# Performance work log

Hardware: AMD Instinct MI355X
Metric: run time of the kernel (lower is better)

Reference implementation:

```python
import jax, jax.numpy as jnp
import numpy as np
import math

B, S, H, NH, HD = 2, 2048, 4096, 32, 128  # batch, seq, hidden, heads, head_dim
ROPE_BASE = 10000.0


def setup_inputs() -> dict:
    key = jax.random.key(0)
    k1, k2 = jax.random.split(key)
    hidden_states = jax.random.normal(k1, (B, S, H), jnp.float32) * 0.02
    W_pack = jax.random.normal(k2, (3 * H, H), jnp.float32) * (1.0 / math.sqrt(H))
    position_ids = jnp.tile(jnp.arange(S, dtype=jnp.int64)[None, :], (B, 1))
    # 4D additive causal mask, as passed by HF Baichuan to this attention module
    causal = jnp.triu(jnp.full((S, S), -1e9, jnp.float32), 1)[None, None, :, :]
    return {"hidden_states": hidden_states, "W_pack": W_pack,
            "attention_mask": causal, "position_ids": position_ids}


def _rope(x, position_ids):
    # x: [B, S, NH, HD]; NeoX-style rotate-half RoPE over full head_dim
    half = HD // 2
    inv_freq = 1.0 / (ROPE_BASE ** (jnp.arange(half, dtype=jnp.float32) / half))
    ang = position_ids.astype(jnp.float32)[:, :, None] * inv_freq  # [B,S,half]
    cos = jnp.concatenate([jnp.cos(ang), jnp.cos(ang)], axis=-1)[:, :, None, :]
    sin = jnp.concatenate([jnp.sin(ang), jnp.sin(ang)], axis=-1)[:, :, None, :]
    x1, x2 = jnp.split(x, 2, axis=-1)
    x_rot = jnp.concatenate([-x2, x1], axis=-1)
    return x * cos + x_rot * sin


def reference(hidden_states, W_pack, attention_mask, position_ids):
    # fused QKV projection (W_pack has no bias in Baichuan)
    proj = hidden_states @ W_pack.T                      # [B,S,3H]
    q, k, v = jnp.split(proj, 3, axis=-1)
    q = q.reshape(B, S, NH, HD)
    k = k.reshape(B, S, NH, HD)
    v = v.reshape(B, S, NH, HD)
    q = _rope(q, position_ids)
    k = _rope(k, position_ids)
    # scaled dot-product attention
    scale = 1.0 / math.sqrt(HD)
    q = q.transpose(0, 2, 1, 3)  # [B,NH,S,HD]
    k = k.transpose(0, 2, 1, 3)
    v = v.transpose(0, 2, 1, 3)
    scores = jnp.einsum("bhqd,bhkd->bhqk", q, k) * scale + attention_mask
    probs = jax.nn.softmax(scores, axis=-1)
    ctx = jnp.einsum("bhqk,bhkd->bhqd", probs, v)        # [B,NH,S,HD]
    attn_output = ctx.transpose(0, 2, 1, 3).reshape(B, S, H)
    return attn_output
```

## Files before the change

kernel.cpp:

```cpp
#include <hip/hip_runtime.h>
#include <hip/hip_bf16.h>
#include <stdint.h>

typedef unsigned short u16;
typedef __attribute__((ext_vector_type(8))) short s16x8;
typedef __attribute__((ext_vector_type(8))) unsigned short u16x8;
typedef __attribute__((ext_vector_type(4))) unsigned short u16x4;
typedef __attribute__((ext_vector_type(4))) float fx4;
typedef __bf16 bf16x8 __attribute__((ext_vector_type(8)));

#define SEQ 2048
#define HID 4096
#define NHEAD 32
#define HDIM 128
#define P3H 12288
#define NKT 64

__device__ __forceinline__ u16 f2bf(float f) {
  unsigned u = __builtin_bit_cast(unsigned, f);
  u += 0x7fffu + ((u >> 16) & 1u);
  return (u16)(u >> 16);
}
__device__ __forceinline__ float bf2f(u16 h) {
  unsigned u = ((unsigned)h) << 16;
  return __builtin_bit_cast(float, u);
}
__device__ __forceinline__ void gload_lds16(const void* g, void* l) {
  __builtin_amdgcn_global_load_lds((const __attribute__((address_space(1))) void*)g,
                                   (__attribute__((address_space(3))) void*)l, 16, 0, 0);
}
__device__ __forceinline__ fx4 mfma16(s16x8 a, s16x8 b, fx4 c) {
  return __builtin_amdgcn_mfma_f32_16x16x32_bf16(
      __builtin_bit_cast(bf16x8, a), __builtin_bit_cast(bf16x8, b), c, 0, 0, 0);
}

__global__ void k_cvt(const float* __restrict__ src, u16* __restrict__ dst, int n4) {
  int i = blockIdx.x * blockDim.x + threadIdx.x;
  if (i >= n4) return;
  float4 v = reinterpret_cast<const float4*>(src)[i];
  u16x4 o;
  o[0] = f2bf(v.x); o[1] = f2bf(v.y); o[2] = f2bf(v.z); o[3] = f2bf(v.w);
  reinterpret_cast<u16x4*>(dst)[i] = o;
}

__device__ __forceinline__ void stage_half(const u16* __restrict__ g, u16* l, int r0, int t) {
#pragma unroll
  for (int c = 0; c < 2; c++) {
    int row = r0 + c * 64 + (t >> 3);
    int blk = (t & 7) ^ ((t >> 3) & 7);
    gload_lds16(g + (size_t)row * HID + blk * 8, l + row * 64 + (t & 7) * 8);
  }
}

#define BAR_OPEN __builtin_amdgcn_s_barrier()
#define BAR_CLOSE do { __builtin_amdgcn_s_barrier(); __builtin_amdgcn_sched_barrier(0); } while (0)
#define LGKM0 do { asm volatile("s_waitcnt lgkmcnt(0)" ::: "memory"); \
                   __builtin_amdgcn_sched_barrier(0); } while (0)

#define LDA_QUAD(qm) do { \
  _Pragma("unroll") for (int mi = 0; mi < 4; mi++) \
  _Pragma("unroll") for (int ks = 0; ks < 2; ks++) { \
    int row = wrr + (qm) * 64 + mi * 16 + li; \
    aA[mi][ks] = *(const s16x8*)&Al[row * 64 + (((ks * 4 + lg) ^ (row & 7)) << 3)]; \
  } } while (0)

#define LDB_QUAD(qn) do { \
  _Pragma("unroll") for (int ni = 0; ni < 2; ni++) \
  _Pragma("unroll") for (int ks = 0; ks < 2; ks++) { \
    int row = wcc + (qn) * 32 + ni * 16 + li; \
    aB[qn][ni][ks] = *(const s16x8*)&Bl[row * 64 + (((ks * 4 + lg) ^ (row & 7)) << 3)]; \
  } } while (0)

#define MMA_QUAD(qm, qn) do { \
  _Pragma("unroll") for (int ks = 0; ks < 2; ks++) \
  _Pragma("unroll") for (int mi = 0; mi < 4; mi++) \
  _Pragma("unroll") for (int ni = 0; ni < 2; ni++) \
    acc[(qm) * 4 + mi][(qn) * 2 + ni] = \
        mfma16(aA[mi][ks], aB[qn][ni][ks], acc[(qm) * 4 + mi][(qn) * 2 + ni]); \
  } while (0)

__global__ void __launch_bounds__(512, 2) k_gemm_qkv(const u16* __restrict__ A,
                                                     const u16* __restrict__ W,
                                                     u16* __restrict__ C) {
  __shared__ u16 SM[2][2][256 * 64];
  const int t = threadIdx.x;
  const int lane = t & 63;
  const int w = t >> 6;
  const int li = lane & 15, lg = lane >> 4;
  const int wr = w >> 2, wc = w & 3;
  const int wrr = wr * 128, wcc = wc * 64;

  const int cpx = gridDim.x >> 3;
  const int swz = (blockIdx.x & 7) * cpx + (blockIdx.x >> 3);
  const int bm = swz / 48, bn = swz - bm * 48;
  const int m0 = bm * 256, n0 = bn * 256;

  const u16* Ag = A + (size_t)m0 * HID;
  const u16* Wg = W + (size_t)n0 * HID;

  fx4 acc[8][4];
#pragma unroll
  for (int i = 0; i < 8; i++)
#pragma unroll
    for (int j = 0; j < 4; j++) acc[i][j] = fx4{0.f, 0.f, 0.f, 0.f};
  s16x8 aA[4][2], aB[2][2][2];

  stage_half(Ag, &SM[0][0][0], 0, t);
  stage_half(Ag, &SM[0][0][0], 128, t);
  stage_half(Wg, &SM[0][1][0], 0, t);
  stage_half(Wg, &SM[0][1][0], 128, t);
  stage_half(Wg + 64, &SM[1][1][0], 0, t);
  stage_half(Wg + 64, &SM[1][1][0], 128, t);
  stage_half(Ag + 64, &SM[1][0][0], 0, t);
  asm volatile("s_waitcnt vmcnt(6)" ::: "memory");
  BAR_CLOSE;

  for (int kt = 0; kt < NKT; kt++) {
    const int cur = kt & 1;
    u16* Al = &SM[cur][0][0];
    u16* Bl = &SM[cur][1][0];
    u16* Anxt = &SM[cur ^ 1][0][0];
    const u16* Ag1 = Ag + (size_t)(kt + 1) * 64;
    const u16* Ag2 = Ag + (size_t)(kt + 2) * 64;
    const u16* Wg2 = Wg + (size_t)(kt + 2) * 64;

    LDA_QUAD(0);
    LDB_QUAD(0);
    if (kt + 1 < NKT) stage_half(Ag1, Anxt, 128, t);
    asm volatile("s_waitcnt lgkmcnt(8)" ::: "memory");
    BAR_OPEN;
    LGKM0;
    __builtin_amdgcn_s_setprio(1);
    MMA_QUAD(0, 0);
    __builtin_amdgcn_s_setprio(0);
    BAR_CLOSE;

    LDB_QUAD(1);
    BAR_OPEN;
    LGKM0;
    __builtin_amdgcn_s_setprio(1);
    MMA_QUAD(0, 1);
    __builtin_amdgcn_s_setprio(0);
    BAR_CLOSE;

    LDA_QUAD(1);
    if (kt + 2 < NKT) stage_half(Wg2, Bl, 0, t);
    BAR_OPEN;
    LGKM0;
    __builtin_amdgcn_s_setprio(1);
    MMA_QUAD(1, 1);
    __builtin_amdgcn_s_setprio(0);
    BAR_CLOSE;

    if (kt + 2 < NKT) {
      stage_half(Wg2, Bl, 128, t);
      stage_half(Ag2, Al, 0, t);
    }
    BAR_OPEN;
    LGKM0;
    __builtin_amdgcn_s_setprio(1);
    MMA_QUAD(1, 0);
    __builtin_amdgcn_s_setprio(0);
    if (kt + 2 < NKT) {
      asm volatile("s_waitcnt vmcnt(6)" ::: "memory");
    } else {
      asm volatile("s_waitcnt vmcnt(0)" ::: "memory");
    }
    BAR_CLOSE;
  }

#pragma unroll
  for (int mi = 0; mi < 8; mi++)
#pragma unroll
    for (int ni = 0; ni < 4; ni++)
#pragma unroll
      for (int j = 0; j < 4; j++) {
        int r = m0 + wrr + mi * 16 + lg * 4 + j;
        int c = n0 + wcc + ni * 16 + li;
        C[(size_t)r * P3H + c] = f2bf(acc[mi][ni][j]);
      }
}

__global__ void k_rope(const u16* __restrict__ proj, u16* __restrict__ q,
                       u16* __restrict__ k, const int* __restrict__ pos_ids) {
  int t = blockIdx.x * 256 + threadIdx.x;
  int d = t & 63;
  int h = (t >> 6) & 31;
  int s = (t >> 11) & 2047;
  int b = t >> 22;
  int prow = b * SEQ + s;
  const u16* pr = proj + (size_t)prow * P3H;
  float q1 = bf2f(pr[h * HDIM + d]);
  float q2 = bf2f(pr[h * HDIM + d + 64]);
  float k1 = bf2f(pr[HID + h * HDIM + d]);
  float k2 = bf2f(pr[HID + h * HDIM + d + 64]);
  float p = (float)pos_ids[prow];
  float invf = exp2f(-(float)d * 0.2076205059304601f);
  float ang = p * invf;
  float sn, cs;
  sincosf(ang, &sn, &cs);
  size_t base = ((size_t)(b * NHEAD + h) * SEQ + s) * HDIM + d;
  q[base]      = f2bf(q1 * cs - q2 * sn);
  q[base + 64] = f2bf(q2 * cs + q1 * sn);
  k[base]      = f2bf(k1 * cs - k2 * sn);
  k[base + 64] = f2bf(k2 * cs + k1 * sn);
}

__global__ void k_vtrans(const u16* __restrict__ proj, u16* __restrict__ vt) {
  int wid = (blockIdx.x * 256 + threadIdx.x) >> 6;
  int lane = threadIdx.x & 63;
  int half = wid & 1;
  int s8 = (wid >> 1) & 255;
  int h = (wid >> 9) & 31;
  int b = wid >> 14;
  int d = half * 64 + lane;
  int s0 = s8 * 8;
  u16x8 v;
#pragma unroll
  for (int r = 0; r < 8; r++)
    v[r] = proj[(size_t)(b * SEQ + s0 + r) * P3H + 2 * HID + h * HDIM + d];
  *reinterpret_cast<u16x8*>(&vt[((size_t)(b * NHEAD + h) * HDIM + d) * SEQ + s0]) = v;
}

__device__ __forceinline__ void stage_kv(const u16* __restrict__ kp, const u16* __restrict__ vp,
                                         u16* ksl, u16* vsl, int kv0, int t) {
#pragma unroll
  for (int c = 0; c < 4; c++) {
    int row = c * 16 + (t >> 4);
    int cb = (t & 15) ^ (row & 7);
    gload_lds16(kp + (size_t)(kv0 + row) * HDIM + cb * 8, ksl + (size_t)(c * 256 + t) * 8);
  }
#pragma unroll
  for (int c = 0; c < 4; c++) {
    int row = c * 32 + (t >> 3);
    int cb = (t & 7) ^ (row & 7);
    gload_lds16(vp + (size_t)row * SEQ + kv0 + cb * 8, vsl + (size_t)(c * 256 + t) * 8);
  }
}

__global__ void __launch_bounds__(256, 2) k_attn(const u16* __restrict__ q,
                                                 const u16* __restrict__ k,
                                                 const u16* __restrict__ vt,
                                                 float* __restrict__ out) {
  __shared__ u16 Ks[2][64 * 128];
  __shared__ u16 Vs[2][128 * 64];
  __shared__ u16 Ps[4][2][16 * 64];
  const int t = threadIdx.x;
  const int w = t >> 6, lane = t & 63;
  const int li = lane & 15, lg = lane >> 4;
  const int qb = gridDim.x - 1 - blockIdx.x;
  const int h = blockIdx.y, b = blockIdx.z;
  const int q0 = qb * 128;
  const int qw = q0 + w * 32;
  const size_t bh = (size_t)(b * NHEAD + h);
  const u16* qp = q + bh * SEQ * HDIM;
  const u16* kp = k + bh * SEQ * HDIM;
  const u16* vp = vt + bh * HDIM * SEQ;

  s16x8 bq[2][4];
#pragma unroll
  for (int g = 0; g < 2; g++)
#pragma unroll
    for (int kk = 0; kk < 4; kk++)
      bq[g][kk] = *reinterpret_cast<const s16x8*>(
          &qp[(size_t)(qw + g * 16 + li) * HDIM + kk * 32 + lg * 8]);

  fx4 Oacc[2][8];
#pragma unroll
  for (int g = 0; g < 2; g++)
#pragma unroll
    for (int nd = 0; nd < 8; nd++) Oacc[g][nd] = fx4{0.f, 0.f, 0.f, 0.f};
  float mrun[2] = {-1e30f, -1e30f}, lrun[2] = {0.f, 0.f};

  const float SC2 = 0.12752551286084110f;
  const float THR = 8.0f / SC2;
  const int nt = 2 * (qb + 1);
  const int psw = (li & 7) << 4;

  stage_kv(kp, vp, Ks[0], Vs[0], 0, t);

  for (int tk = 0; tk < nt; tk++) {
    const int cur = tk & 1;
    if (tk + 1 < nt) {
      stage_kv(kp, vp, Ks[cur ^ 1], Vs[cur ^ 1], (tk + 1) * 64, t);
      asm volatile("s_waitcnt vmcnt(8)" ::: "memory");
    } else {
      asm volatile("s_waitcnt vmcnt(0)" ::: "memory");
    }
    __builtin_amdgcn_s_barrier();

    const u16* Kc = Ks[cur];
    const u16* Vc = Vs[cur];
    const int kv0 = tk * 64;
    const bool diag = (tk >= 2 * qb);

    fx4 sc[2][4];
#pragma unroll
    for (int g = 0; g < 2; g++)
#pragma unroll
      for (int n = 0; n < 4; n++) sc[g][n] = fx4{0.f, 0.f, 0.f, 0.f};
    __builtin_amdgcn_s_setprio(1);
#pragma unroll
    for (int n = 0; n < 4; n++) {
      int r = n * 16 + li;
#pragma unroll
      for (int kk = 0; kk < 4; kk++) {
        s16x8 ak = *reinterpret_cast<const s16x8*>(
            &Kc[r * 128 + (((kk * 4 + lg) ^ (r & 7)) << 3)]);
        sc[0][n] = mfma16(ak, bq[0][kk], sc[0][n]);
        sc[1][n] = mfma16(ak, bq[1][kk], sc[1][n]);
      }
    }
    __builtin_amdgcn_s_setprio(0);

    if (diag) {
#pragma unroll
      for (int g = 0; g < 2; g++) {
        const int qg = qw + g * 16 + li;
#pragma unroll
        for (int n = 0; n < 4; n++)
#pragma unroll
          for (int j = 0; j < 4; j++) {
            int kvg = kv0 + n * 16 + lg * 4 + j;
            if (kvg > qg) sc[g][n][j] = -1e30f;
          }
      }
    }

    s16x8 ap[2][2];
#pragma unroll
    for (int g = 0; g < 2; g++) {
      float mn[4];
#pragma unroll
      for (int n = 0; n < 4; n++)
        mn[n] = fmaxf(fmaxf(sc[g][n][0], sc[g][n][1]), fmaxf(sc[g][n][2], sc[g][n][3]));
      float vmax = fmaxf(fmaxf(mn[0], mn[1]), fmaxf(mn[2], mn[3]));
      vmax = fmaxf(vmax, __shfl_xor(vmax, 16));
      vmax = fmaxf(vmax, __shfl_xor(vmax, 32));
      if (__any(vmax > mrun[g] + THR)) {
        float mnew = fmaxf(mrun[g], vmax);
        float al = exp2f((mrun[g] - mnew) * SC2);
        mrun[g] = mnew;
        lrun[g] *= al;
        float alj[4];
#pragma unroll
        for (int j = 0; j < 4; j++) alj[j] = __shfl(al, lg * 4 + j);
#pragma unroll
        for (int nd = 0; nd < 8; nd++)
#pragma unroll
          for (int j = 0; j < 4; j++) Oacc[g][nd][j] *= alj[j];
      }
      const float mS = mrun[g] * SC2;
      float ps[4];
#pragma unroll
      for (int n = 0; n < 4; n++) {
        u16x4 pk;
        float pv0 = exp2f(__builtin_fmaf(sc[g][n][0], SC2, -mS));
        float pv1 = exp2f(__builtin_fmaf(sc[g][n][1], SC2, -mS));
        float pv2 = exp2f(__builtin_fmaf(sc[g][n][2], SC2, -mS));
        float pv3 = exp2f(__builtin_fmaf(sc[g][n][3], SC2, -mS));
        pk[0] = __builtin_bit_cast(u16, __float2bfloat16(pv0));
        pk[1] = __builtin_bit_cast(u16, __float2bfloat16(pv1));
        pk[2] = __builtin_bit_cast(u16, __float2bfloat16(pv2));
        pk[3] = __builtin_bit_cast(u16, __float2bfloat16(pv3));
        ps[n] = (pv0 + pv1) + (pv2 + pv3);
        *reinterpret_cast<u16x4*>(
            &Ps[w][g][li * 64 + (((n * 32 + lg * 8) ^ psw) >> 1)]) = pk;
      }
      float psum = (ps[0] + ps[1]) + (ps[2] + ps[3]);
      psum += __shfl_xor(psum, 16);
      psum += __shfl_xor(psum, 32);
      lrun[g] += psum;
#pragma unroll
      for (int kvc = 0; kvc < 2; kvc++)
        ap[g][kvc] = *reinterpret_cast<const s16x8*>(
            &Ps[w][g][li * 64 + (((kvc * 64 + lg * 16) ^ psw) >> 1)]);
    }

    __builtin_amdgcn_s_setprio(1);
#pragma unroll
    for (int nd = 0; nd < 8; nd++) {
      int dr = nd * 16 + li;
#pragma unroll
      for (int kvc = 0; kvc < 2; kvc++) {
        s16x8 bv = *reinterpret_cast<const s16x8*>(
            &Vc[dr * 64 + (((kvc * 4 + lg) ^ (dr & 7)) << 3)]);
        Oacc[0][nd] = mfma16(ap[0][kvc], bv, Oacc[0][nd]);
        Oacc[1][nd] = mfma16(ap[1][kvc], bv, Oacc[1][nd]);
      }
    }
    __builtin_amdgcn_s_setprio(0);

    __builtin_amdgcn_s_barrier();
    __builtin_amdgcn_sched_barrier(0);
  }

#pragma unroll
  for (int g = 0; g < 2; g++)
#pragma unroll
    for (int j = 0; j < 4; j++) {
      float rl = 1.0f / __shfl(lrun[g], lg * 4 + j);
      int s = qw + g * 16 + lg * 4 + j;
      float* op = out + ((size_t)(b * SEQ) + s) * HID + h * HDIM;
#pragma unroll
      for (int nd = 0; nd < 8; nd++) op[nd * 16 + li] = Oacc[g][nd][j] * rl;
    }
}

extern "C" void kernel_launch(void* const* d_in, const int* in_sizes, int n_in,
                              void* d_out, int out_size, void* d_ws, size_t ws_size,
                              hipStream_t stream) {
  const float* hidden = (const float*)d_in[0];
  const float* wpack = (const float*)d_in[1];
  const int* pos = (const int*)d_in[3];
  float* out = (float*)d_out;

  char* ws = (char*)d_ws;
  u16* hid_bf = (u16*)ws;
  u16* wp_bf = (u16*)(ws + ((size_t)32 << 20));
  u16* qb = (u16*)ws;
  u16* kb = (u16*)(ws + ((size_t)32 << 20));
  u16* vtb = (u16*)(ws + ((size_t)64 << 20));
  u16* proj = (u16*)(ws + ((size_t)128 << 20));

  k_cvt<<<(HID * HID / 4 + 255) / 256, 256, 0, stream>>>(hidden, hid_bf, HID * HID / 4);
  k_cvt<<<(P3H * HID / 4 + 255) / 256, 256, 0, stream>>>(wpack, wp_bf, P3H * HID / 4);

  k_gemm_qkv<<<768, 512, 0, stream>>>(hid_bf, wp_bf, proj);

  k_rope<<<(2 * SEQ * NHEAD * 64) / 256, 256, 0, stream>>>(proj, qb, kb, pos);
  k_vtrans<<<(2 * NHEAD * (SEQ / 8) * 2) / 4, 256, 0, stream>>>(proj, vtb);

  dim3 ga(SEQ / 128, NHEAD, 2);
  k_attn<<<ga, 256, 0, stream>>>(qb, kb, vtb, out);
}
```

Before: 645.7 us.

## Read K/V directly from global in attention, reorder grid, retime GEMM A prefetch

The attention kernel drops its double-buffered LDS staging of K and V and its barriers. Each wave now loads its MFMA operands straight from global memory, relying on L1/L2 cache reuse. The grid is reordered so blocks sharing a batch-head launch adjacently, and the GEMM prologue/loop moves the A-tile prefetch one step later with adjusted vmcnt waits. This removes LDS traffic and sync but exposes global-load latency inside the MFMA loops and duplicates K/V reads across the four waves.

```diff
diff --git a/kernel.cpp b/kernel.cpp
--- a/kernel.cpp
+++ b/kernel.cpp
@@ -105,14 +105,13 @@
     for (int j = 0; j < 4; j++) acc[i][j] = fx4{0.f, 0.f, 0.f, 0.f};
   s16x8 aA[4][2], aB[2][2][2];
 
+  stage_half(Wg, &SM[0][1][0], 0, t);
+  stage_half(Wg, &SM[0][1][0], 128, t);
   stage_half(Ag, &SM[0][0][0], 0, t);
   stage_half(Ag, &SM[0][0][0], 128, t);
-  stage_half(Wg, &SM[0][1][0], 0, t);
-  stage_half(Wg, &SM[0][1][0], 128, t);
   stage_half(Wg + 64, &SM[1][1][0], 0, t);
   stage_half(Wg + 64, &SM[1][1][0], 128, t);
-  stage_half(Ag + 64, &SM[1][0][0], 0, t);
-  asm volatile("s_waitcnt vmcnt(6)" ::: "memory");
+  asm volatile("s_waitcnt vmcnt(4)" ::: "memory");
   BAR_CLOSE;
 
   for (int kt = 0; kt < NKT; kt++) {
@@ -120,13 +119,12 @@
     u16* Al = &SM[cur][0][0];
     u16* Bl = &SM[cur][1][0];
     u16* Anxt = &SM[cur ^ 1][0][0];
-    const u16* Ag1 = Ag + (size_t)(kt + 1) * 64;
-    const u16* Ag2 = Ag + (size_t)(kt + 2) * 64;
-    const u16* Wg2 = Wg + (size_t)(kt + 2) * 64;
+    const u16* Agn = Ag + (size_t)(kt + 1) * 64;
+    const u16* Wgn = Wg + (size_t)(kt + 2) * 64;
 
     LDA_QUAD(0);
     LDB_QUAD(0);
-    if (kt + 1 < NKT) stage_half(Ag1, Anxt, 128, t);
+    if (kt + 1 < NKT) stage_half(Agn, Anxt, 0, t);
     asm volatile("s_waitcnt lgkmcnt(8)" ::: "memory");
     BAR_OPEN;
     LGKM0;
@@ -136,6 +134,7 @@
     BAR_CLOSE;
 
     LDB_QUAD(1);
+    if (kt + 1 < NKT) stage_half(Agn, Anxt, 128, t);
     BAR_OPEN;
     LGKM0;
     __builtin_amdgcn_s_setprio(1);
@@ -144,7 +143,7 @@
     BAR_CLOSE;
 
     LDA_QUAD(1);
-    if (kt + 2 < NKT) stage_half(Wg2, Bl, 0, t);
+    if (kt + 2 < NKT) stage_half(Wgn, Bl, 0, t);
     BAR_OPEN;
     LGKM0;
     __builtin_amdgcn_s_setprio(1);
@@ -152,17 +151,14 @@
     __builtin_amdgcn_s_setprio(0);
     BAR_CLOSE;
 
-    if (kt + 2 < NKT) {
-      stage_half(Wg2, Bl, 128, t);
-      stage_half(Ag2, Al, 0, t);
-    }
+    if (kt + 2 < NKT) stage_half(Wgn, Bl, 128, t);
     BAR_OPEN;
     LGKM0;
     __builtin_amdgcn_s_setprio(1);
     MMA_QUAD(1, 0);
     __builtin_amdgcn_s_setprio(0);
     if (kt + 2 < NKT) {
-      asm volatile("s_waitcnt vmcnt(6)" ::: "memory");
+      asm volatile("s_waitcnt vmcnt(4)" ::: "memory");
     } else {
       asm volatile("s_waitcnt vmcnt(0)" ::: "memory");
     }
@@ -222,40 +218,20 @@
   *reinterpret_cast<u16x8*>(&vt[((size_t)(b * NHEAD + h) * HDIM + d) * SEQ + s0]) = v;
 }
 
-__device__ __forceinline__ void stage_kv(const u16* __restrict__ kp, const u16* __restrict__ vp,
-                                         u16* ksl, u16* vsl, int kv0, int t) {
-#pragma unroll
-  for (int c = 0; c < 4; c++) {
-    int row = c * 16 + (t >> 4);
-    int cb = (t & 15) ^ (row & 7);
-    gload_lds16(kp + (size_t)(kv0 + row) * HDIM + cb * 8, ksl + (size_t)(c * 256 + t) * 8);
-  }
-#pragma unroll
-  for (int c = 0; c < 4; c++) {
-    int row = c * 32 + (t >> 3);
-    int cb = (t & 7) ^ (row & 7);
-    gload_lds16(vp + (size_t)row * SEQ + kv0 + cb * 8, vsl + (size_t)(c * 256 + t) * 8);
-  }
-}
-
-__global__ void __launch_bounds__(256, 2) k_attn(const u16* __restrict__ q,
-                                                 const u16* __restrict__ k,
-                                                 const u16* __restrict__ vt,
-                                                 float* __restrict__ out) {
-  __shared__ u16 Ks[2][64 * 128];
-  __shared__ u16 Vs[2][128 * 64];
+__global__ void __launch_bounds__(256) k_attn(const u16* __restrict__ q,
+                                              const u16* __restrict__ k,
+                                              const u16* __restrict__ vt,
+                                              float* __restrict__ out) {
   __shared__ u16 Ps[4][2][16 * 64];
   const int t = threadIdx.x;
   const int w = t >> 6, lane = t & 63;
   const int li = lane & 15, lg = lane >> 4;
-  const int qb = gridDim.x - 1 - blockIdx.x;
-  const int h = blockIdx.y, b = blockIdx.z;
-  const int q0 = qb * 128;
-  const int qw = q0 + w * 32;
-  const size_t bh = (size_t)(b * NHEAD + h);
-  const u16* qp = q + bh * SEQ * HDIM;
-  const u16* kp = k + bh * SEQ * HDIM;
-  const u16* vp = vt + bh * HDIM * SEQ;
+  const int bh = blockIdx.x;
+  const int qb = (gridDim.y - 1) - blockIdx.y;
+  const int qw = qb * 128 + w * 32;
+  const u16* qp = q + (size_t)bh * SEQ * HDIM;
+  const u16* kp = k + (size_t)bh * SEQ * HDIM;
+  const u16* vp = vt + (size_t)bh * HDIM * SEQ;
 
   s16x8 bq[2][4];
 #pragma unroll
@@ -277,20 +253,7 @@
   const int nt = 2 * (qb + 1);
   const int psw = (li & 7) << 4;
 
-  stage_kv(kp, vp, Ks[0], Vs[0], 0, t);
-
   for (int tk = 0; tk < nt; tk++) {
-    const int cur = tk & 1;
-    if (tk + 1 < nt) {
-      stage_kv(kp, vp, Ks[cur ^ 1], Vs[cur ^ 1], (tk + 1) * 64, t);
-      asm volatile("s_waitcnt vmcnt(8)" ::: "memory");
-    } else {
-      asm volatile("s_waitcnt vmcnt(0)" ::: "memory");
-    }
-    __builtin_amdgcn_s_barrier();
-
-    const u16* Kc = Ks[cur];
-    const u16* Vc = Vs[cur];
     const int kv0 = tk * 64;
     const bool diag = (tk >= 2 * qb);
 
@@ -302,11 +265,10 @@
     __builtin_amdgcn_s_setprio(1);
 #pragma unroll
     for (int n = 0; n < 4; n++) {
-      int r = n * 16 + li;
+      const u16* krow = kp + (size_t)(kv0 + n * 16 + li) * HDIM + lg * 8;
 #pragma unroll
       for (int kk = 0; kk < 4; kk++) {
-        s16x8 ak = *reinterpret_cast<const s16x8*>(
-            &Kc[r * 128 + (((kk * 4 + lg) ^ (r & 7)) << 3)]);
+        s16x8 ak = *reinterpret_cast<const s16x8*>(krow + kk * 32);
         sc[0][n] = mfma16(ak, bq[0][kk], sc[0][n]);
         sc[1][n] = mfma16(ak, bq[1][kk], sc[1][n]);
       }
@@ -380,19 +342,15 @@
     __builtin_amdgcn_s_setprio(1);
 #pragma unroll
     for (int nd = 0; nd < 8; nd++) {
-      int dr = nd * 16 + li;
+      const u16* vrow = vp + (size_t)(nd * 16 + li) * SEQ + kv0 + lg * 8;
 #pragma unroll
       for (int kvc = 0; kvc < 2; kvc++) {
-        s16x8 bv = *reinterpret_cast<const s16x8*>(
-            &Vc[dr * 64 + (((kvc * 4 + lg) ^ (dr & 7)) << 3)]);
+        s16x8 bv = *reinterpret_cast<const s16x8*>(vrow + kvc * 32);
         Oacc[0][nd] = mfma16(ap[0][kvc], bv, Oacc[0][nd]);
         Oacc[1][nd] = mfma16(ap[1][kvc], bv, Oacc[1][nd]);
       }
     }
     __builtin_amdgcn_s_setprio(0);
-
-    __builtin_amdgcn_s_barrier();
-    __builtin_amdgcn_sched_barrier(0);
   }
 
 #pragma unroll
@@ -401,7 +359,7 @@
     for (int j = 0; j < 4; j++) {
       float rl = 1.0f / __shfl(lrun[g], lg * 4 + j);
       int s = qw + g * 16 + lg * 4 + j;
-      float* op = out + ((size_t)(b * SEQ) + s) * HID + h * HDIM;
+      float* op = out + ((size_t)((bh >> 5) * SEQ) + s) * HID + (bh & 31) * HDIM;
 #pragma unroll
       for (int nd = 0; nd < 8; nd++) op[nd * 16 + li] = Oacc[g][nd][j] * rl;
     }
@@ -431,6 +389,6 @@
   k_rope<<<(2 * SEQ * NHEAD * 64) / 256, 256, 0, stream>>>(proj, qb, kb, pos);
   k_vtrans<<<(2 * NHEAD * (SEQ / 8) * 2) / 4, 256, 0, stream>>>(proj, vtb);
 
-  dim3 ga(SEQ / 128, NHEAD, 2);
+  dim3 ga(2 * NHEAD, SEQ / 128);
   k_attn<<<ga, 256, 0, stream>>>(qb, kb, vtb, out);
 }
```

Measured after the change: 785.8 us. 1.22x slower.
